# Optimization experiments

Hardware: AMD Instinct MI355X
Metric: run time of the kernel (lower is better)

## Reference

```python
import jax, jax.numpy as jnp
import numpy as np

AZ = -999999.0  # ALMOST_ZERO_LOG_SCALE
N = 100000      # nodes
E = N - 1       # tree edges
D = 768         # input_dim
H = 256         # hidden_dim
C = 16          # num_classes


def setup_inputs() -> dict:
    key = jax.random.key(0)
    ks = jax.random.split(key, 14)
    scale = 0.02
    features = jax.random.normal(ks[0], (N, D), dtype=jnp.float32)
    # tree edges: child i (1..N-1) has parent sampled from [0, N)
    parent_idx = jax.random.randint(ks[1], (E,), 0, N, dtype=jnp.int32)
    child_idx = jnp.arange(1, N, dtype=jnp.int32)
    label_observed = jax.random.randint(ks[2], (N,), 0, 2, dtype=jnp.int32)
    true_labels = jax.random.randint(ks[3], (N,), 0, C, dtype=jnp.int32)
    # MLP feature extractor (num_layers=2, Linear+ReLU each, feature_extractor=True)
    W1 = jax.random.normal(ks[4], (D, H), dtype=jnp.float32) * scale
    b1 = jnp.zeros((H,), dtype=jnp.float32)
    W2 = jax.random.normal(ks[5], (H, H), dtype=jnp.float32) * scale
    b2 = jnp.zeros((H,), dtype=jnp.float32)
    # build_unary_potentials: Linear(H, C)
    Wu = jax.random.normal(ks[6], (H, C), dtype=jnp.float32) * scale
    bu = jnp.zeros((C,), dtype=jnp.float32)
    # build_edge_potentials: Linear(2H, C*C)
    We = jax.random.normal(ks[7], (2 * H, C * C), dtype=jnp.float32) * scale
    be = jnp.zeros((C * C,), dtype=jnp.float32)
    return {
        "features": features, "parent_idx": parent_idx, "child_idx": child_idx,
        "label_observed": label_observed, "true_labels": true_labels,
        "W1": W1, "b1": b1, "W2": W2, "b2": b2,
        "Wu": Wu, "bu": bu, "We": We, "be": be,
    }


def reference(features, parent_idx, child_idx, label_observed, true_labels,
              W1, b1, W2, b2, Wu, bu, We, be):
    obs = label_observed.astype(bool)
    # MLP feature extractor over all nodes at once (original loops per-node)
    h = jax.nn.relu(features @ W1 + b1)
    h = jax.nn.relu(h @ W2 + b2)                      # [N, H]
    # unary potentials; observed nodes get 0 at true label, AZ elsewhere
    unary_pred = h @ Wu + bu                          # [N, C]
    lbl = jnp.arange(C, dtype=true_labels.dtype)
    obs_unary = jnp.where(true_labels[:, None] == lbl[None, :], 0.0, AZ)
    unary = jnp.where(obs[:, None], obs_unary, unary_pred)  # [N, C]
    # edge potentials: Linear on concat(parent_hidden, child_hidden)
    hp = h[parent_idx]                                # [E, H]
    hc = h[child_idx]                                 # [E, H]
    ep = (jnp.concatenate([hp, hc], axis=1) @ We + be).reshape(E, C, C)
    pl = true_labels[parent_idx]                      # [E]
    cl = true_labels[child_idx]                       # [E]
    op = obs[parent_idx]                              # [E]
    oc = obs[child_idx]                               # [E]
    row = lbl[None, :, None]                          # broadcast over rows
    col = lbl[None, None, :]                          # broadcast over cols
    # both observed: 0 at [parent_label, child_label], AZ elsewhere
    allow_both = (row == pl[:, None, None]) & (col == cl[:, None, None])
    both = (op & oc)[:, None, None]
    # child-only observed: keep row at child label; parent-only: keep col at parent label
    keep = (((oc & ~op)[:, None, None] & (row == cl[:, None, None]))
            | ((op & ~oc)[:, None, None] & (col == pl[:, None, None]))
            | (~op & ~oc)[:, None, None])
    ep_masked = jnp.where(both,
                          jnp.where(allow_both, 0.0, AZ),
                          jnp.where(keep, ep, ep + AZ))
    return unary, ep_masked
```

## Files before the change

kernel.cpp:

```cpp
#include <hip/hip_runtime.h>
#include <cstddef>

#define AZ -999999.0f

typedef float  f32x4  __attribute__((ext_vector_type(4)));
typedef short  s16x8  __attribute__((ext_vector_type(8)));
typedef __bf16 bf16x8 __attribute__((ext_vector_type(8)));

__device__ __forceinline__ unsigned short f2bf(float f) {
    union { float f; unsigned u; } un; un.f = f;
    return (unsigned short)((un.u + 0x7FFFu + ((un.u >> 16) & 1u)) >> 16);
}

__device__ __forceinline__ f32x4 mfma16(s16x8 a, s16x8 b, f32x4 c) {
    return __builtin_amdgcn_mfma_f32_16x16x32_bf16(
        __builtin_bit_cast(bf16x8, a), __builtin_bit_cast(bf16x8, b), c, 0, 0, 0);
}

__device__ __forceinline__ void gl2lds16(const void* g, void* l) {
    __builtin_amdgcn_global_load_lds(
        (const __attribute__((address_space(1))) unsigned int*)g,
        (__attribute__((address_space(3))) unsigned int*)l, 16, 0, 0);
}

__global__ void transpose_cvt(const float* __restrict__ B,
                              unsigned short* __restrict__ BT, int K) {
    int idx = blockIdx.x * 256 + threadIdx.x;
    int k = idx >> 8, n = idx & 255;
    BT[(size_t)n * K + k] = f2bf(B[idx]);
}

__global__ void edge_meta_kernel(const int* __restrict__ pidx, const int* __restrict__ cidx,
                                 const int* __restrict__ tl, const int* __restrict__ obs,
                                 int* __restrict__ meta, int E) {
    int e = blockIdx.x * 256 + threadIdx.x;
    if (e < E) {
        int p = pidx[e], c = cidx[e];
        meta[e] = (tl[p] & 15) | ((tl[c] & 15) << 4) | ((obs[p] & 1) << 8) | ((obs[c] & 1) << 9);
    }
}

template<int AMODE, int EPI>
__global__ __launch_bounds__(256) void gemm_kernel(
    const void* __restrict__ Aptr, const unsigned short* __restrict__ BT,
    const float* __restrict__ bias, void* __restrict__ outp,
    int M, int K,
    const int* __restrict__ parent_idx, const int* __restrict__ child_idx,
    const int* __restrict__ meta)
{
    constexpr int ABYTES = (AMODE == 0) ? 16384 : 8192;
    __shared__ __align__(16) char smem[ABYTES + 8192];
    float*          Asf = (float*)smem;
    unsigned short* Ash = (unsigned short*)smem;
    unsigned short* Bsh = (unsigned short*)(smem + ABYTES);

    const int tid  = threadIdx.x;
    const int lane = tid & 63, wave = tid >> 6;
    const int row0    = blockIdx.y * 128;
    const int colbase = blockIdx.x * 128;
    const int wr = (wave >> 1) * 64, wc = (wave & 1) * 64;
    const int quad = lane >> 4, l16 = lane & 15;

    const int sub4 = lane >> 2, c4 = lane & 3;
    const int gcB  = c4 ^ ((sub4 >> 1) & 3);
    size_t b_off[2]; unsigned lds_b[2];
#pragma unroll
    for (int j = 0; j < 2; ++j) {
        int r = wave * 32 + j * 16 + sub4;
        b_off[j] = (size_t)(colbase + r) * K + gcB * 8;
        lds_b[j] = (unsigned)(wave * 32 + j * 16) * 64;
    }
    const int sub8 = lane >> 3, c8 = lane & 7;
    size_t a_off[4]; unsigned lds_a[4];
    int pn[2], cn[2];
    if constexpr (AMODE == 0) {
        const int gcA = c8 ^ sub8;
#pragma unroll
        for (int j = 0; j < 4; ++j) {
            int r  = wave * 32 + j * 8 + sub8;
            int gr = row0 + r; if (gr > M - 1) gr = M - 1;
            a_off[j] = (size_t)gr * K + gcA * 4;
            lds_a[j] = (unsigned)(wave * 32 + j * 8) * 128;
        }
    } else {
        const int gcA = c4 ^ ((sub4 >> 1) & 3);
#pragma unroll
        for (int j = 0; j < 2; ++j) {
            int r  = wave * 32 + j * 16 + sub4;
            int gr = row0 + r; if (gr > M - 1) gr = M - 1;
            if constexpr (AMODE == 2) { pn[j] = parent_idx[gr]; cn[j] = child_idx[gr]; }
            a_off[j] = (size_t)gr * K + gcA * 8;
            lds_a[j] = (unsigned)(wave * 32 + j * 16) * 64;
        }
        if constexpr (AMODE == 2) { a_off[0] = gcA * 8; a_off[1] = gcA * 8; }
    }

    const f32x4 fz = {0.f, 0.f, 0.f, 0.f};
    f32x4 acc[4][4];
#pragma unroll
    for (int i = 0; i < 4; ++i)
#pragma unroll
        for (int j = 0; j < 4; ++j) acc[i][j] = fz;

    const unsigned short* Abh = (const unsigned short*)Aptr;
    const float*          Af  = (const float*)Aptr;

    const int nkt = K >> 5;
    for (int kt = 0; kt < nkt; ++kt) {
        const int kbase = kt << 5;
        if constexpr (AMODE == 0) {
#pragma unroll
            for (int j = 0; j < 4; ++j)
                gl2lds16(Af + a_off[j] + kbase, smem + lds_a[j]);
        } else if constexpr (AMODE == 1) {
#pragma unroll
            for (int j = 0; j < 2; ++j)
                gl2lds16(Abh + a_off[j] + kbase, smem + lds_a[j]);
        } else {
#pragma unroll
            for (int j = 0; j < 2; ++j) {
                int node = (kbase < 256) ? pn[j] : cn[j];
                gl2lds16(Abh + (size_t)node * 256 + (kbase & 255) + a_off[j],
                         smem + lds_a[j]);
            }
        }
#pragma unroll
        for (int j = 0; j < 2; ++j)
            gl2lds16(BT + b_off[j] + kbase, (char*)Bsh + lds_b[j]);

        __syncthreads();

        s16x8 af[4], bf[4];
        if constexpr (AMODE == 0) {
            const int s = l16 & 7;
            const int c0 = (2 * quad) ^ s, c1 = c0 ^ 1;
#pragma unroll
            for (int f = 0; f < 4; ++f) {
                int row = wr + f * 16 + l16;
                f32x4 v0 = *(const f32x4*)&Asf[row * 32 + c0 * 4];
                f32x4 v1 = *(const f32x4*)&Asf[row * 32 + c1 * 4];
                s16x8 a;
                a[0] = (short)f2bf(v0[0]); a[1] = (short)f2bf(v0[1]);
                a[2] = (short)f2bf(v0[2]); a[3] = (short)f2bf(v0[3]);
                a[4] = (short)f2bf(v1[0]); a[5] = (short)f2bf(v1[1]);
                a[6] = (short)f2bf(v1[2]); a[7] = (short)f2bf(v1[3]);
                af[f] = a;
            }
        } else {
            const int ca = quad ^ ((l16 >> 1) & 3);
#pragma unroll
            for (int f = 0; f < 4; ++f)
                af[f] = *(const s16x8*)&Ash[(wr + f * 16 + l16) * 32 + ca * 8];
        }
        {
            const int cb = quad ^ ((l16 >> 1) & 3);
#pragma unroll
            for (int f = 0; f < 4; ++f)
                bf[f] = *(const s16x8*)&Bsh[(wc + f * 16 + l16) * 32 + cb * 8];
        }
#pragma unroll
        for (int fr = 0; fr < 4; ++fr)
#pragma unroll
            for (int fc = 0; fc < 4; ++fc)
                acc[fr][fc] = mfma16(af[fr], bf[fc], acc[fr][fc]);
        __syncthreads();
    }

    float bv[4];
#pragma unroll
    for (int fc = 0; fc < 4; ++fc) bv[fc] = bias[colbase + wc + fc * 16 + l16];

    if constexpr (EPI == 0) {
        unsigned short* out = (unsigned short*)outp;
#pragma unroll
        for (int fr = 0; fr < 4; ++fr) {
#pragma unroll
            for (int r = 0; r < 4; ++r) {
                int gr = row0 + wr + fr * 16 + quad * 4 + r;
                if (gr < M) {
#pragma unroll
                    for (int fc = 0; fc < 4; ++fc) {
                        float v = acc[fr][fc][r] + bv[fc];
                        v = v > 0.f ? v : 0.f;
                        out[(size_t)gr * 256 + colbase + wc + fc * 16 + l16] = f2bf(v);
                    }
                }
            }
        }
    } else {
        float* out = (float*)outp;
#pragma unroll
        for (int fr = 0; fr < 4; ++fr) {
#pragma unroll
            for (int r = 0; r < 4; ++r) {
                int e = row0 + wr + fr * 16 + quad * 4 + r;
                if (e < M) {
                    int m  = meta[e];
                    int pl = m & 15, cl = (m >> 4) & 15;
                    int op = (m >> 8) & 1, oc = (m >> 9) & 1;
#pragma unroll
                    for (int fc = 0; fc < 4; ++fc) {
                        int n = colbase + wc + fc * 16 + l16;
                        float v = acc[fr][fc][r] + bv[fc];
                        int rr = n >> 4, cc = n & 15;
                        if (op & oc)  v = (rr == pl && cc == cl) ? 0.0f : AZ;
                        else if (oc)  { if (rr != cl) v += AZ; }
                        else if (op)  { if (cc != pl) v += AZ; }
                        out[(size_t)e * 256 + n] = v;
                    }
                }
            }
        }
    }
}

__global__ __launch_bounds__(256) void unary_kernel(
    const unsigned short* __restrict__ h2, const float* __restrict__ Wu,
    const float* __restrict__ bu, const int* __restrict__ tl,
    const int* __restrict__ obs, float* __restrict__ out, int N)
{
    __shared__ unsigned short WuT[16][272];
    const int tid = threadIdx.x;
    {
        const f32x4* wrow = (const f32x4*)&Wu[tid * 16];
        float tmp[16];
#pragma unroll
        for (int j = 0; j < 4; ++j) {
            f32x4 v = wrow[j];
            tmp[j * 4 + 0] = v[0]; tmp[j * 4 + 1] = v[1];
            tmp[j * 4 + 2] = v[2]; tmp[j * 4 + 3] = v[3];
        }
#pragma unroll
        for (int c = 0; c < 16; ++c) WuT[c][tid] = f2bf(tmp[c]);
    }
    __syncthreads();
    const int lane = tid & 63, wave = tid >> 6;
    const int quad = lane >> 4, col = lane & 15;
    const int n0 = blockIdx.x * 64 + wave * 16;
    int arow = n0 + col;
    if (arow > N - 1) arow = N - 1;
    f32x4 acc = {0.f, 0.f, 0.f, 0.f};
#pragma unroll
    for (int kt = 0; kt < 8; ++kt) {
        s16x8 a = *(const s16x8*)&h2[(size_t)arow * 256 + kt * 32 + quad * 8];
        s16x8 b = *(const s16x8*)&WuT[col][kt * 32 + quad * 8];
        acc = mfma16(a, b, acc);
    }
    float bvc = bu[col];
#pragma unroll
    for (int r = 0; r < 4; ++r) {
        int node = n0 + quad * 4 + r;
        if (node < N) {
            float v = obs[node] ? ((tl[node] == col) ? 0.0f : AZ) : (acc[r] + bvc);
            out[(size_t)node * 16 + col] = v;
        }
    }
}

extern "C" void kernel_launch(void* const* d_in, const int* in_sizes, int n_in,
                              void* d_out, int out_size, void* d_ws, size_t ws_size,
                              hipStream_t stream) {
    const float* features = (const float*)d_in[0];
    const int* parent_idx = (const int*)d_in[1];
    const int* child_idx  = (const int*)d_in[2];
    const int* label_obs  = (const int*)d_in[3];
    const int* true_lab   = (const int*)d_in[4];
    const float* W1 = (const float*)d_in[5];
    const float* b1 = (const float*)d_in[6];
    const float* W2 = (const float*)d_in[7];
    const float* b2 = (const float*)d_in[8];
    const float* Wu = (const float*)d_in[9];
    const float* bu = (const float*)d_in[10];
    const float* We = (const float*)d_in[11];
    const float* be = (const float*)d_in[12];
    float* out = (float*)d_out;

    const int N = 100000, E = N - 1;

    char* ws = (char*)d_ws;
    unsigned short* h1  = (unsigned short*)ws;
    unsigned short* h2  = (unsigned short*)(ws + (size_t)N * 256 * 2);
    unsigned short* W1T = (unsigned short*)(ws + (size_t)N * 256 * 4);
    unsigned short* W2T = W1T + 768 * 256;
    unsigned short* WeT = W2T + 256 * 256;
    int*            meta = (int*)(WeT + 512 * 256);

    transpose_cvt<<<768, 256, 0, stream>>>(W1, W1T, 768);
    transpose_cvt<<<256, 256, 0, stream>>>(W2, W2T, 256);
    transpose_cvt<<<512, 256, 0, stream>>>(We, WeT, 512);
    edge_meta_kernel<<<(E + 255) / 256, 256, 0, stream>>>(parent_idx, child_idx,
                                                          true_lab, label_obs, meta, E);

    dim3 gn(2, (N + 127) / 128);
    gemm_kernel<0, 0><<<gn, 256, 0, stream>>>(features, W1T, b1, h1, N, 768,
                                              nullptr, nullptr, nullptr);
    gemm_kernel<1, 0><<<gn, 256, 0, stream>>>(h1, W2T, b2, h2, N, 256,
                                              nullptr, nullptr, nullptr);
    unary_kernel<<<(N + 63) / 64, 256, 0, stream>>>(h2, Wu, bu, true_lab, label_obs, out, N);
    dim3 ge(2, (E + 127) / 128);
    gemm_kernel<2, 1><<<ge, 256, 0, stream>>>(h2, WeT, be, out + (size_t)N * 16, E, 512,
                                              parent_idx, child_idx, meta);
}
```

Baseline: 650.1 us.

## Fuse second MLP layer with unary head and merge setup kernels

New measurement: 640.2 us. Within noise of the previous version (-1.5%).

```diff
diff --git a/kernel.cpp b/kernel.cpp
--- a/kernel.cpp
+++ b/kernel.cpp
@@ -6,6 +6,7 @@
 typedef float  f32x4  __attribute__((ext_vector_type(4)));
 typedef short  s16x8  __attribute__((ext_vector_type(8)));
 typedef __bf16 bf16x8 __attribute__((ext_vector_type(8)));
+typedef unsigned short ushort_t;
 
 __device__ __forceinline__ unsigned short f2bf(float f) {
     union { float f; unsigned u; } un; un.f = f;
@@ -23,26 +24,41 @@
         (__attribute__((address_space(3))) unsigned int*)l, 16, 0, 0);
 }
 
-__global__ void transpose_cvt(const float* __restrict__ B,
-                              unsigned short* __restrict__ BT, int K) {
-    int idx = blockIdx.x * 256 + threadIdx.x;
-    int k = idx >> 8, n = idx & 255;
-    BT[(size_t)n * K + k] = f2bf(B[idx]);
-}
-
-__global__ void edge_meta_kernel(const int* __restrict__ pidx, const int* __restrict__ cidx,
-                                 const int* __restrict__ tl, const int* __restrict__ obs,
-                                 int* __restrict__ meta, int E) {
-    int e = blockIdx.x * 256 + threadIdx.x;
-    if (e < E) {
-        int p = pidx[e], c = cidx[e];
-        meta[e] = (tl[p] & 15) | ((tl[c] & 15) << 4) | ((obs[p] & 1) << 8) | ((obs[c] & 1) << 9);
+__global__ void setup_kernel(
+    const float* __restrict__ W1, const float* __restrict__ W2,
+    const float* __restrict__ We, const float* __restrict__ Wu,
+    ushort_t* __restrict__ W1T, ushort_t* __restrict__ W2T,
+    ushort_t* __restrict__ WeT, ushort_t* __restrict__ WuTs,
+    const int* __restrict__ pidx, const int* __restrict__ cidx,
+    const int* __restrict__ tl, const int* __restrict__ obs,
+    int* __restrict__ meta, int E)
+{
+    int b = blockIdx.x, t = threadIdx.x;
+    if (b < 768) {
+        int idx = b * 256 + t; int k = idx >> 8, n = idx & 255;
+        W1T[(size_t)n * 768 + k] = f2bf(W1[idx]);
+    } else if (b < 1024) {
+        int idx = (b - 768) * 256 + t; int k = idx >> 8, n = idx & 255;
+        W2T[n * 256 + k] = f2bf(W2[idx]);
+    } else if (b < 1536) {
+        int idx = (b - 1024) * 256 + t; int k = idx >> 8, n = idx & 255;
+        WeT[(size_t)n * 512 + k] = f2bf(We[idx]);
+    } else if (b < 1552) {
+        int idx = (b - 1536) * 256 + t; int k = idx >> 4, c = idx & 15;
+        WuTs[c * 256 + (((k >> 3) ^ (c & 7)) << 3) + (k & 7)] = f2bf(Wu[idx]);
+    } else {
+        int e = (b - 1552) * 256 + t;
+        if (e < E) {
+            int p = pidx[e], c = cidx[e];
+            meta[e] = (tl[p] & 15) | ((tl[c] & 15) << 4)
+                    | ((obs[p] & 1) << 8) | ((obs[c] & 1) << 9);
+        }
     }
 }
 
 template<int AMODE, int EPI>
 __global__ __launch_bounds__(256) void gemm_kernel(
-    const void* __restrict__ Aptr, const unsigned short* __restrict__ BT,
+    const void* __restrict__ Aptr, const ushort_t* __restrict__ BT,
     const float* __restrict__ bias, void* __restrict__ outp,
     int M, int K,
     const int* __restrict__ parent_idx, const int* __restrict__ child_idx,
@@ -50,9 +66,9 @@
 {
     constexpr int ABYTES = (AMODE == 0) ? 16384 : 8192;
     __shared__ __align__(16) char smem[ABYTES + 8192];
-    float*          Asf = (float*)smem;
-    unsigned short* Ash = (unsigned short*)smem;
-    unsigned short* Bsh = (unsigned short*)(smem + ABYTES);
+    float*    Asf = (float*)smem;
+    ushort_t* Ash = (ushort_t*)smem;
+    ushort_t* Bsh = (ushort_t*)(smem + ABYTES);
 
     const int tid  = threadIdx.x;
     const int lane = tid & 63, wave = tid >> 6;
@@ -102,8 +118,8 @@
 #pragma unroll
         for (int j = 0; j < 4; ++j) acc[i][j] = fz;
 
-    const unsigned short* Abh = (const unsigned short*)Aptr;
-    const float*          Af  = (const float*)Aptr;
+    const ushort_t* Abh = (const ushort_t*)Aptr;
+    const float*    Af  = (const float*)Aptr;
 
     const int nkt = K >> 5;
     for (int kt = 0; kt < nkt; ++kt) {
@@ -112,10 +128,6 @@
 #pragma unroll
             for (int j = 0; j < 4; ++j)
                 gl2lds16(Af + a_off[j] + kbase, smem + lds_a[j]);
-        } else if constexpr (AMODE == 1) {
-#pragma unroll
-            for (int j = 0; j < 2; ++j)
-                gl2lds16(Abh + a_off[j] + kbase, smem + lds_a[j]);
         } else {
 #pragma unroll
             for (int j = 0; j < 2; ++j) {
@@ -171,7 +183,7 @@
     for (int fc = 0; fc < 4; ++fc) bv[fc] = bias[colbase + wc + fc * 16 + l16];
 
     if constexpr (EPI == 0) {
-        unsigned short* out = (unsigned short*)outp;
+        ushort_t* out = (ushort_t*)outp;
 #pragma unroll
         for (int fr = 0; fr < 4; ++fr) {
 #pragma unroll
@@ -214,45 +226,122 @@
     }
 }
 
-__global__ __launch_bounds__(256) void unary_kernel(
-    const unsigned short* __restrict__ h2, const float* __restrict__ Wu,
+__global__ __launch_bounds__(256) void gemm2_unary_kernel(
+    const ushort_t* __restrict__ h1, const ushort_t* __restrict__ W2T,
+    const float* __restrict__ b2, const ushort_t* __restrict__ WuTs,
     const float* __restrict__ bu, const int* __restrict__ tl,
-    const int* __restrict__ obs, float* __restrict__ out, int N)
+    const int* __restrict__ obs, ushort_t* __restrict__ h2,
+    float* __restrict__ out_unary, int N)
 {
-    __shared__ unsigned short WuT[16][272];
-    const int tid = threadIdx.x;
+    __shared__ __align__(16) char smem[4096 + 16384 + 32768 + 8192];
+    ushort_t* Ash = (ushort_t*)smem;
+    ushort_t* Bsh = (ushort_t*)(smem + 4096);
+    ushort_t* Hsh = (ushort_t*)(smem + 20480);
+    ushort_t* Wsh = (ushort_t*)(smem + 53248);
+
+    const int tid = threadIdx.x, lane = tid & 63, wave = tid >> 6;
+    const int quad = lane >> 4, l16 = lane & 15;
+    const int sub4 = lane >> 2, c4 = lane & 3;
+    const int n0 = blockIdx.x * 64;
+    const int wc = wave * 64;
+
+#pragma unroll
+    for (int j = 0; j < 2; ++j)
+        gl2lds16(WuTs + j * 2048 + wave * 512 + lane * 8,
+                 (char*)Wsh + j * 4096 + wave * 1024);
+
+    const int gcA = c4 ^ ((sub4 >> 1) & 3);
+    int gra = n0 + wave * 16 + sub4; if (gra > N - 1) gra = N - 1;
+    const size_t a_goff = (size_t)gra * 256 + gcA * 8;
+    const unsigned a_loff = (unsigned)wave * 1024;
+    size_t b_goff[4]; unsigned b_loff[4];
+#pragma unroll
+    for (int j = 0; j < 4; ++j) {
+        int nrow = j * 64 + wave * 16 + sub4;
+        b_goff[j] = (size_t)nrow * 256 + gcA * 8;
+        b_loff[j] = (unsigned)(j * 64 + wave * 16) * 64;
+    }
+
+    const f32x4 fz = {0.f, 0.f, 0.f, 0.f};
+    f32x4 acc[4][4];
+#pragma unroll
+    for (int i = 0; i < 4; ++i)
+#pragma unroll
+        for (int j = 0; j < 4; ++j) acc[i][j] = fz;
+
+    for (int kt = 0; kt < 8; ++kt) {
+        const int kbase = kt << 5;
+        gl2lds16(h1 + a_goff + kbase, smem + a_loff);
+#pragma unroll
+        for (int j = 0; j < 4; ++j)
+            gl2lds16(W2T + b_goff[j] + kbase, (char*)Bsh + b_loff[j]);
+        __syncthreads();
+        const int cs = quad ^ ((l16 >> 1) & 3);
+        s16x8 af[4], bf[4];
+#pragma unroll
+        for (int f = 0; f < 4; ++f)
+            af[f] = *(const s16x8*)&Ash[(f * 16 + l16) * 32 + cs * 8];
+#pragma unroll
+        for (int f = 0; f < 4; ++f)
+            bf[f] = *(const s16x8*)&Bsh[(wc + f * 16 + l16) * 32 + cs * 8];
+#pragma unroll
+        for (int fr = 0; fr < 4; ++fr)
+#pragma unroll
+            for (int fc = 0; fc < 4; ++fc)
+                acc[fr][fc] = mfma16(af[fr], bf[fc], acc[fr][fc]);
+        __syncthreads();
+    }
+
+    float bv[4];
+#pragma unroll
+    for (int fc = 0; fc < 4; ++fc) bv[fc] = b2[wc + fc * 16 + l16];
+#pragma unroll
+    for (int fr = 0; fr < 4; ++fr) {
+#pragma unroll
+        for (int r = 0; r < 4; ++r) {
+            int row = fr * 16 + quad * 4 + r;
+#pragma unroll
+            for (int fc = 0; fc < 4; ++fc) {
+                int col = wc + fc * 16 + l16;
+                float v = acc[fr][fc][r] + bv[fc];
+                v = v > 0.f ? v : 0.f;
+                Hsh[row * 256 + (((col >> 3) ^ (row & 7)) << 3) + (col & 7)] = f2bf(v);
+            }
+        }
+    }
+    __syncthreads();
+
     {
-        const f32x4* wrow = (const f32x4*)&Wu[tid * 16];
-        float tmp[16];
-#pragma unroll
-        for (int j = 0; j < 4; ++j) {
-            f32x4 v = wrow[j];
-            tmp[j * 4 + 0] = v[0]; tmp[j * 4 + 1] = v[1];
-            tmp[j * 4 + 2] = v[2]; tmp[j * 4 + 3] = v[3];
-        }
-#pragma unroll
-        for (int c = 0; c < 16; ++c) WuT[c][tid] = f2bf(tmp[c]);
-    }
-    __syncthreads();
-    const int lane = tid & 63, wave = tid >> 6;
-    const int quad = lane >> 4, col = lane & 15;
-    const int n0 = blockIdx.x * 64 + wave * 16;
-    int arow = n0 + col;
-    if (arow > N - 1) arow = N - 1;
-    f32x4 acc = {0.f, 0.f, 0.f, 0.f};
-#pragma unroll
-    for (int kt = 0; kt < 8; ++kt) {
-        s16x8 a = *(const s16x8*)&h2[(size_t)arow * 256 + kt * 32 + quad * 8];
-        s16x8 b = *(const s16x8*)&WuT[col][kt * 32 + quad * 8];
-        acc = mfma16(a, b, acc);
-    }
-    float bvc = bu[col];
-#pragma unroll
-    for (int r = 0; r < 4; ++r) {
-        int node = n0 + quad * 4 + r;
-        if (node < N) {
-            float v = obs[node] ? ((tl[node] == col) ? 0.0f : AZ) : (acc[r] + bvc);
-            out[(size_t)node * 16 + col] = v;
+        int row = tid >> 2, cc = tid & 3;
+        int gr = n0 + row;
+        if (gr < N) {
+#pragma unroll
+            for (int j = 0; j < 8; ++j) {
+                int phys = (j * 4 + cc) ^ (row & 7);
+                s16x8 v = *(const s16x8*)&Hsh[row * 256 + phys * 8];
+                *(s16x8*)&h2[(size_t)gr * 256 + (j * 4 + cc) * 8] = v;
+            }
+        }
+    }
+
+    {
+        const int arow = wave * 16 + l16;
+        f32x4 accu = fz;
+#pragma unroll
+        for (int kt = 0; kt < 8; ++kt) {
+            int pc = (kt * 4 + quad) ^ (l16 & 7);
+            s16x8 a = *(const s16x8*)&Hsh[arow * 256 + pc * 8];
+            s16x8 b = *(const s16x8*)&Wsh[l16 * 256 + pc * 8];
+            accu = mfma16(a, b, accu);
+        }
+        float bvc = bu[l16];
+#pragma unroll
+        for (int r = 0; r < 4; ++r) {
+            int node = n0 + wave * 16 + quad * 4 + r;
+            if (node < N) {
+                float v = obs[node] ? ((tl[node] == l16) ? 0.0f : AZ) : (accu[r] + bvc);
+                out_unary[(size_t)node * 16 + l16] = v;
+            }
         }
     }
 }
@@ -278,25 +367,23 @@
     const int N = 100000, E = N - 1;
 
     char* ws = (char*)d_ws;
-    unsigned short* h1  = (unsigned short*)ws;
-    unsigned short* h2  = (unsigned short*)(ws + (size_t)N * 256 * 2);
-    unsigned short* W1T = (unsigned short*)(ws + (size_t)N * 256 * 4);
-    unsigned short* W2T = W1T + 768 * 256;
-    unsigned short* WeT = W2T + 256 * 256;
-    int*            meta = (int*)(WeT + 512 * 256);
-
-    transpose_cvt<<<768, 256, 0, stream>>>(W1, W1T, 768);
-    transpose_cvt<<<256, 256, 0, stream>>>(W2, W2T, 256);
-    transpose_cvt<<<512, 256, 0, stream>>>(We, WeT, 512);
-    edge_meta_kernel<<<(E + 255) / 256, 256, 0, stream>>>(parent_idx, child_idx,
-                                                          true_lab, label_obs, meta, E);
+    ushort_t* h1   = (ushort_t*)ws;
+    ushort_t* h2   = (ushort_t*)(ws + (size_t)N * 256 * 2);
+    ushort_t* W1T  = (ushort_t*)(ws + (size_t)N * 256 * 4);
+    ushort_t* W2T  = W1T + 768 * 256;
+    ushort_t* WeT  = W2T + 256 * 256;
+    ushort_t* WuTs = WeT + 512 * 256;
+    int*      meta = (int*)(WuTs + 16 * 256);
+
+    setup_kernel<<<1943, 256, 0, stream>>>(W1, W2, We, Wu, W1T, W2T, WeT, WuTs,
+                                           parent_idx, child_idx, true_lab, label_obs,
+                                           meta, E);
 
     dim3 gn(2, (N + 127) / 128);
     gemm_kernel<0, 0><<<gn, 256, 0, stream>>>(features, W1T, b1, h1, N, 768,
                                               nullptr, nullptr, nullptr);
-    gemm_kernel<1, 0><<<gn, 256, 0, stream>>>(h1, W2T, b2, h2, N, 256,
-                                              nullptr, nullptr, nullptr);
-    unary_kernel<<<(N + 63) / 64, 256, 0, stream>>>(h2, Wu, bu, true_lab, label_obs, out, N);
+    gemm2_unary_kernel<<<(N + 63) / 64, 256, 0, stream>>>(h1, W2T, b2, WuTs, bu,
+                                                          true_lab, label_obs, h2, out, N);
     dim3 ge(2, (E + 127) / 128);
     gemm_kernel<2, 1><<<ge, 256, 0, stream>>>(h2, WeT, be, out + (size_t)N * 16, E, 512,
                                               parent_idx, child_idx, meta);
```
